# Kernel tuning notes

Measured on AMD Instinct MI355X. Metric: run time of the kernel, lower is better.

The kernel has to match this reference:

```python
import jax, jax.numpy as jnp
import numpy as np
from jax import lax

B = 32          # batch
L = 12          # n_blocks
HD = 768        # hidden_d
NH = 12         # n_heads
DH = HD // NH   # d_head = 64
NP = 14         # n_patches per side
S = NP * NP + 1 # seq len = 197
IN_D = 32 * 25  # 800, conv channels * 5x5 patch
OUT = 1000
EPS = 1e-5


def setup_inputs() -> dict:
    key = jax.random.key(0)
    ks = jax.random.split(key, 10)
    r = lambda k, s: jax.random.normal(k, s, jnp.float32) * 0.02
    return {
        "images": jax.random.normal(ks[0], (B, 3, 280, 280), jnp.float32),
        "conv_w": r(ks[1], (32, 3, 5, 5)),
        "conv_b": jnp.zeros((32,), jnp.float32),
        "bn_g": jnp.ones((32,), jnp.float32),
        "bn_b": jnp.zeros((32,), jnp.float32),
        "bn_m": jnp.zeros((32,), jnp.float32),
        "bn_v": jnp.ones((32,), jnp.float32),
        "map_w": r(ks[2], (HD, IN_D)),
        "map_b": jnp.zeros((HD,), jnp.float32),
        "cls_tok": jax.random.uniform(ks[3], (1, HD), jnp.float32),
        "ln_g": jnp.ones((L, HD), jnp.float32),
        "ln_b": jnp.zeros((L, HD), jnp.float32),
        "wq": r(ks[4], (L, NH, DH, DH)), "bq": jnp.zeros((L, NH, DH), jnp.float32),
        "wk": r(ks[5], (L, NH, DH, DH)), "bk": jnp.zeros((L, NH, DH), jnp.float32),
        "wv": r(ks[6], (L, NH, DH, DH)), "bv": jnp.zeros((L, NH, DH), jnp.float32),
        "mlp_w": r(ks[7], (OUT, HD)),
        "mlp_b": jnp.zeros((OUT,), jnp.float32),
    }


def _pos_emb(s, d):
    # pe[i,j] = sin(i/10000^(j/d)) if j even else cos(i/10000^((j-1)/d))
    i = jnp.arange(s, dtype=jnp.float32)[:, None]
    j = jnp.arange(d)[None, :]
    jf = j.astype(jnp.float32)
    ang_even = i / (10000.0 ** (jf / d))
    ang_odd = i / (10000.0 ** ((jf - 1.0) / d))
    return jnp.where(j % 2 == 0, jnp.sin(ang_even), jnp.cos(ang_odd))


def reference(images, conv_w, conv_b, bn_g, bn_b, bn_m, bn_v, map_w, map_b,
              cls_tok, ln_g, ln_b, wq, bq, wk, bk, wv, bv, mlp_w, mlp_b):
    # patch-embed conv: (B,3,280,280) -> (B,32,70,70)
    x = lax.conv_general_dilated(images, conv_w, (4, 4), [(1, 1), (1, 1)],
                                 dimension_numbers=('NCHW', 'OIHW', 'NCHW'))
    x = x + conv_b[None, :, None, None]
    # BatchNorm (eval) + ReLU; Dropout is identity in eval
    x = (x - bn_m[None, :, None, None]) * (bn_g / jnp.sqrt(bn_v + EPS))[None, :, None, None] \
        + bn_b[None, :, None, None]
    x = jax.nn.relu(x)
    n = x.shape[0]
    # split into 5x5 patches: (n,32,70,70) -> (n,196,800)
    x = x.reshape(n, 32, NP, 5, NP, 5).transpose(0, 2, 4, 1, 3, 5).reshape(n, NP * NP, IN_D)
    tok = x @ map_w.T + map_b                                   # (n,196,768)
    tok = jnp.concatenate([jnp.broadcast_to(cls_tok[None], (n, 1, HD)), tok], axis=1)
    out = tok + _pos_emb(S, HD)[None]                           # (n,197,768)
    scale = 1.0 / jnp.sqrt(jnp.float32(DH))
    for l in range(L):
        # LayerNorm
        mu = out.mean(-1, keepdims=True)
        var = out.var(-1, keepdims=True)
        h = (out - mu) / jnp.sqrt(var + EPS) * ln_g[l] + ln_b[l]
        xh = h.reshape(n, S, NH, DH)
        q = jnp.einsum('nshd,hed->nshe', xh, wq[l]) + bq[l]
        k = jnp.einsum('nshd,hed->nshe', xh, wk[l]) + bk[l]
        v = jnp.einsum('nshd,hed->nshe', xh, wv[l]) + bv[l]
        attn = jax.nn.softmax(jnp.einsum('nshe,nthe->nhst', q, k) * scale, axis=-1)
        o = jnp.einsum('nhst,nthe->nshe', attn, v).reshape(n, S, HD)
        out = out + o  # residual; NOTE: source block has no MLP sublayer
    cls = out[:, 0]
    return jax.nn.softmax(cls @ mlp_w.T + mlp_b, axis=-1)
```

## Files before the change

kernel.cpp:

```cpp
#include <hip/hip_runtime.h>

#define BB 32
#define LLAYERS 12
#define HDIM 768
#define NHEAD 12
#define DHEAD 64
#define SEQ 197
#define IND 800
#define NOUT 1000
#define EPSF 1e-5f
#define NTOK (BB * SEQ)
#define NPATCH (BB * 196)
#define SCALE 0.125f

typedef __attribute__((ext_vector_type(4))) float f32x4;
typedef __attribute__((ext_vector_type(8))) short short8;

static __device__ __forceinline__ ushort f2bf(float f) {
    union { float f; unsigned u; } v; v.f = f;
    unsigned r = v.u + 0x7FFFu + ((v.u >> 16) & 1u);
    return (ushort)(r >> 16);
}

static __device__ __forceinline__ void gload_lds16(const void* g, void* l) {
    __builtin_amdgcn_global_load_lds(
        (const __attribute__((address_space(1))) void*)g,
        (__attribute__((address_space(3))) void*)l, 16, 0, 0);
}

__global__ __launch_bounds__(256) void k_cvt(
    const float* __restrict__ s, ushort* __restrict__ d, int n4)
{
    int i = blockIdx.x * 256 + threadIdx.x;
    if (i < n4) {
        float4 v = *(const float4*)&s[i * 4];
        ushort4 u = {f2bf(v.x), f2bf(v.y), f2bf(v.z), f2bf(v.w)};
        *(ushort4*)&d[i * 4] = u;
    }
}

__global__ __launch_bounds__(256) void k_cvtw(
    const float* __restrict__ wq, const float* __restrict__ wk,
    const float* __restrict__ wv, ushort* __restrict__ dst)
{
    int t = blockIdx.x * 256 + threadIdx.x;
    if (t >= 3 * 144 * 512) return;
    int lane = t & 63;
    int rest = t >> 6;
    int ktnt = rest & 7;
    int mlh = rest >> 3;
    int h = mlh % 12, ml = mlh / 12;
    int l = ml % 12, m = ml / 12;
    int nt = ktnt & 3, kt = ktnt >> 2;
    int e = nt * 16 + (lane & 15);
    int d = kt * 32 + (lane >> 4) * 8;
    const float* src = ((m == 0) ? wq : (m == 1) ? wk : wv)
                       + (((long)l * 12 + h) * 64 + e) * 64 + d;
    float4 a = *(const float4*)src;
    float4 b = *(const float4*)(src + 4);
    short8 u;
    u[0] = (short)f2bf(a.x); u[1] = (short)f2bf(a.y);
    u[2] = (short)f2bf(a.z); u[3] = (short)f2bf(a.w);
    u[4] = (short)f2bf(b.x); u[5] = (short)f2bf(b.y);
    u[6] = (short)f2bf(b.z); u[7] = (short)f2bf(b.w);
    *(short8*)&dst[(long)mlh * 4096 + ktnt * 512 + lane * 8] = u;
}

__global__ __launch_bounds__(256) void k_pos(float* __restrict__ pos)
{
    int s = blockIdx.x;
    for (int e = threadIdx.x; e < HDIM; e += 256) {
        float freq = expf((float)(e & ~1) * (-9.210340371976184f / 768.0f));
        float ang = (float)s * freq;
        pos[s * HDIM + e] = (e & 1) ? cosf(ang) : sinf(ang);
    }
}

__global__ __launch_bounds__(320) void k_conv_patch(
    const float* __restrict__ img, const float* __restrict__ cw,
    const float* __restrict__ cb, const float* __restrict__ bg,
    const float* __restrict__ bbias, const float* __restrict__ bm,
    const float* __restrict__ bvv, ushort* __restrict__ X)
{
    __shared__ float tile[2][3][21][21];
    __shared__ float w[2400];
    __shared__ float scale[32], shift[32];
    int tid = threadIdx.x;

    for (int i = tid; i < 2400; i += 320) w[i] = cw[i];
    if (tid < 32) {
        float sc = bg[tid] * rsqrtf(bvv[tid] + EPSF);
        scale[tid] = sc;
        shift[tid] = (cb[tid] - bm[tid]) * sc + bbias[tid];
    }
    for (int i = tid; i < 2 * 3 * 441; i += 320) {
        int pp = i / 1323, j = i % 1323;
        int c = j / 441, r = (j / 21) % 21, cc = j % 21;
        int gp = blockIdx.x * 2 + pp;
        int n = gp / 196, p = gp % 196;
        int h0 = (p / 14) * 20 - 1, w0 = (p % 14) * 20 - 1;
        int gh = h0 + r, gw = w0 + cc;
        float v = 0.f;
        if (gh >= 0 && gh < 280 && gw >= 0 && gw < 280)
            v = img[((long)(n * 3 + c) * 280 + gh) * 280 + gw];
        tile[pp][c][r][cc] = v;
    }
    __syncthreads();

    int pp = tid / 160, u = tid % 160;
    int c = u / 5, ph = u % 5;
    float acc[5] = {0.f, 0.f, 0.f, 0.f, 0.f};
    const float* wp = &w[c * 75];
    #pragma unroll
    for (int ci = 0; ci < 3; ci++) {
        #pragma unroll
        for (int kh = 0; kh < 5; kh++) {
            const float* row = &tile[pp][ci][ph * 4 + kh][0];
            float rv[21];
            #pragma unroll
            for (int j = 0; j < 21; j++) rv[j] = row[j];
            #pragma unroll
            for (int kw = 0; kw < 5; kw++) {
                float wv = wp[ci * 25 + kh * 5 + kw];
                #pragma unroll
                for (int pw = 0; pw < 5; pw++)
                    acc[pw] += rv[pw * 4 + kw] * wv;
            }
        }
    }
    int gp = blockIdx.x * 2 + pp;
    long ob = (long)gp * 800 + c * 25 + ph * 5;
    #pragma unroll
    for (int pw = 0; pw < 5; pw++) {
        float val = acc[pw] * scale[c] + shift[c];
        X[ob + pw] = f2bf(fmaxf(val, 0.f));
    }
}

__global__ void k_cls(const float* __restrict__ cls_tok,
                      const float* __restrict__ pos, float* __restrict__ tok)
{
    int n = blockIdx.x, tid = threadIdx.x;
    for (int e = tid; e < HDIM; e += 256)
        tok[(long)n * SEQ * HDIM + e] = cls_tok[e] + pos[e];
}

__global__ __launch_bounds__(256, 2) void k_embed(
    const ushort* __restrict__ Xg, const ushort* __restrict__ Wg,
    const float* __restrict__ bias, const float* __restrict__ pos,
    float* __restrict__ tok)
{
    __shared__ __align__(16) ushort As[128 * 32];
    __shared__ __align__(16) ushort Bs[64 * 32];
    int m0 = blockIdx.x * 128, e0 = blockIdx.y * 64;
    int tid = threadIdx.x, lane = tid & 63, wave = tid >> 6;
    int col = lane & 15, quad = lane >> 4;
    int wm = (wave & 1) * 64, wn = (wave >> 1) * 32;
    int lr = lane >> 2, lc = (lane & 3) * 8;
    f32x4 zero4 = {0.f, 0.f, 0.f, 0.f};
    f32x4 acc[4][2];
    #pragma unroll
    for (int mt = 0; mt < 4; mt++)
        #pragma unroll
        for (int nt = 0; nt < 2; nt++) acc[mt][nt] = zero4;

    for (int k0 = 0; k0 < 800; k0 += 32) {
        __syncthreads();
        #pragma unroll
        for (int i = 0; i < 2; i++) {
            int c = wave * 2 + i;
            gload_lds16(&Xg[(long)(m0 + c * 16 + lr) * 800 + k0 + lc], &As[c * 512]);
        }
        {
            int c = wave;
            gload_lds16(&Wg[(long)(e0 + c * 16 + lr) * 800 + k0 + lc], &Bs[c * 512]);
        }
        __syncthreads();
        short8 a[4], b[2];
        #pragma unroll
        for (int mt = 0; mt < 4; mt++)
            a[mt] = *(const short8*)&As[(wm + mt * 16 + col) * 32 + quad * 8];
        #pragma unroll
        for (int nt = 0; nt < 2; nt++)
            b[nt] = *(const short8*)&Bs[(wn + nt * 16 + col) * 32 + quad * 8];
        #pragma unroll
        for (int mt = 0; mt < 4; mt++)
            #pragma unroll
            for (int nt = 0; nt < 2; nt++)
                acc[mt][nt] = __builtin_amdgcn_mfma_f32_16x16x32_bf16(a[mt], b[nt], acc[mt][nt], 0, 0, 0);
    }
    #pragma unroll
    for (int mt = 0; mt < 4; mt++) {
        #pragma unroll
        for (int r = 0; r < 4; r++) {
            int m = m0 + wm + mt * 16 + quad * 4 + r;
            int n = m / 196, s = m - n * 196 + 1;
            long rowb = ((long)n * SEQ + s) * HDIM;
            #pragma unroll
            for (int nt = 0; nt < 2; nt++) {
                int e = e0 + wn + nt * 16 + col;
                tok[rowb + e] = acc[mt][nt][r] + bias[e] + pos[s * HDIM + e];
            }
        }
    }
}

__global__ __launch_bounds__(256) void k_lnstats0(
    const float* __restrict__ tok, float* __restrict__ stats_out)
{
    int tid = threadIdx.x, lane = tid & 63, wave = tid >> 6;
    int row = blockIdx.x * 4 + wave;
    const float* p = tok + (long)row * HDIM;
    float s = 0.f, sq = 0.f;
    #pragma unroll
    for (int k = 0; k < 3; k++) {
        float4 v = *(const float4*)&p[k * 256 + lane * 4];
        s += v.x + v.y + v.z + v.w;
        sq += v.x * v.x + v.y * v.y + v.z * v.z + v.w * v.w;
    }
    #pragma unroll
    for (int off = 1; off < 64; off <<= 1) {
        s += __shfl_xor(s, off);
        sq += __shfl_xor(sq, off);
    }
    float* sp = &stats_out[(long)row * 24];
    if (lane == 0) { sp[0] = s; sp[1] = sq; }
    if (lane >= 2 && lane < 24) sp[lane] = 0.f;
}

__global__ __launch_bounds__(512, 1) void k_layer(
    float* __restrict__ tok,
    const float* __restrict__ stats_in, float* __restrict__ stats_out,
    const float* __restrict__ lng, const float* __restrict__ lnb,
    const ushort* __restrict__ wqs, const float* __restrict__ bqp,
    const ushort* __restrict__ wks, const float* __restrict__ bkp,
    const ushort* __restrict__ wvs, const float* __restrict__ bvp)
{
    __shared__ __align__(16) ushort Wl[3][4096];
    __shared__ __align__(16) ushort xh[208 * 72];
    __shared__ __align__(16) ushort Ks[208 * 72];
    __shared__ __align__(16) ushort Vt[64 * 232];
    __shared__ __align__(16) ushort Ps[8][16 * 40];
    __shared__ float smu[208], srstd[208];
    __shared__ float bias[3][64];

    int h = blockIdx.x, n = blockIdx.y;
    int tid = threadIdx.x, lane = tid & 63, wave = tid >> 6;
    int col = lane & 15, quad = lane >> 4;
    f32x4 zero4 = {0.f, 0.f, 0.f, 0.f};

    const ushort* wsz0 = wqs + (long)h * 4096;
    const ushort* wsz1 = wks + (long)h * 4096;
    const ushort* wsz2 = wvs + (long)h * 4096;
    {
        int c = wave;
        gload_lds16(&wsz0[c * 512 + lane * 8], &Wl[0][c * 512]);
        gload_lds16(&wsz1[c * 512 + lane * 8], &Wl[1][c * 512]);
        gload_lds16(&wsz2[c * 512 + lane * 8], &Wl[2][c * 512]);
    }
    if (tid < 192) {
        int m = tid >> 6, e = tid & 63;
        bias[m][e] = ((m == 0) ? bqp : (m == 1) ? bkp : bvp)[h * 64 + e];
    }
    for (int r = tid; r < SEQ; r += 512) {
        const float* sp = &stats_in[((long)n * SEQ + r) * 24];
        float s = 0.f, sq = 0.f;
        #pragma unroll
        for (int j = 0; j < 6; j++) {
            float4 v = *(const float4*)&sp[j * 4];
            s += v.x + v.z;
            sq += v.y + v.w;
        }
        float mu = s / 768.f;
        smu[r] = mu;
        srstd[r] = rsqrtf(sq / 768.f - mu * mu + EPSF);
    }
    for (int i = tid; i < 64 * 24; i += 512) {
        int e = i / 24, t = 208 + i % 24;
        Vt[e * 232 + t] = 0;
    }
    __syncthreads();

    for (int i = tid; i < 208 * 16; i += 512) {
        int r = i >> 4, c4 = i & 15;
        ushort4 u = {0, 0, 0, 0};
        if (r < SEQ) {
            float4 v = *(const float4*)&tok[((long)n * SEQ + r) * HDIM + h * 64 + c4 * 4];
            float mu = smu[r], rstd = srstd[r];
            int d = c4 * 4;
            const float* g = &lng[h * 64 + d];
            const float* bb = &lnb[h * 64 + d];
            u.x = f2bf((v.x - mu) * rstd * g[0] + bb[0]);
            u.y = f2bf((v.y - mu) * rstd * g[1] + bb[1]);
            u.z = f2bf((v.z - mu) * rstd * g[2] + bb[2]);
            u.w = f2bf((v.w - mu) * rstd * g[3] + bb[3]);
        }
        *(ushort4*)&xh[r * 72 + c4 * 4] = u;
    }
    __syncthreads();

    #pragma unroll
    for (int sl = 0; sl < 2; sl++) {
        int st = sl * 8 + wave;
        if (st < 13) {
            int q0 = st * 16;
            short8 a[2];
            a[0] = *(const short8*)&xh[(q0 + col) * 72 + quad * 8];
            a[1] = *(const short8*)&xh[(q0 + col) * 72 + 32 + quad * 8];
            #pragma unroll
            for (int m = 0; m < 3; m++) {
                f32x4 acc[4] = {zero4, zero4, zero4, zero4};
                #pragma unroll
                for (int kt = 0; kt < 2; kt++)
                    #pragma unroll
                    for (int nt = 0; nt < 4; nt++) {
                        short8 b = *(const short8*)&Wl[m][(kt * 4 + nt) * 512 + lane * 8];
                        acc[nt] = __builtin_amdgcn_mfma_f32_16x16x32_bf16(a[kt], b, acc[nt], 0, 0, 0);
                    }
                if (m == 0) {
                    #pragma unroll
                    for (int nt = 0; nt < 4; nt++)
                        #pragma unroll
                        for (int r = 0; r < 4; r++)
                            xh[(q0 + quad * 4 + r) * 72 + nt * 16 + col] =
                                f2bf(acc[nt][r] + bias[0][nt * 16 + col]);
                } else if (m == 1) {
                    #pragma unroll
                    for (int nt = 0; nt < 4; nt++)
                        #pragma unroll
                        for (int r = 0; r < 4; r++)
                            Ks[(q0 + quad * 4 + r) * 72 + nt * 16 + col] =
                                f2bf(acc[nt][r] + bias[1][nt * 16 + col]);
                } else {
                    #pragma unroll
                    for (int nt = 0; nt < 4; nt++)
                        #pragma unroll
                        for (int r = 0; r < 4; r++)
                            Vt[(nt * 16 + col) * 232 + q0 + quad * 4 + r] =
                                f2bf(acc[nt][r] + bias[2][nt * 16 + col]);
                }
            }
        }
    }
    __syncthreads();

    ushort* myP = &Ps[wave][0];
    #pragma unroll
    for (int sl = 0; sl < 2; sl++) {
        int st = sl * 8 + wave;
        if (st >= 13) continue;
        int q0 = st * 16;
        short8 aq[2];
        aq[0] = *(const short8*)&xh[(q0 + col) * 72 + quad * 8];
        aq[1] = *(const short8*)&xh[(q0 + col) * 72 + 32 + quad * 8];

        f32x4 sc[13];
        #pragma unroll
        for (int tt = 0; tt < 13; tt++) sc[tt] = zero4;
        #pragma unroll
        for (int tt = 0; tt < 13; tt++) {
            #pragma unroll
            for (int dt = 0; dt < 2; dt++) {
                short8 bk = *(const short8*)&Ks[(tt * 16 + col) * 72 + dt * 32 + quad * 8];
                sc[tt] = __builtin_amdgcn_mfma_f32_16x16x32_bf16(aq[dt], bk, sc[tt], 0, 0, 0);
            }
        }

        float rinv[4];
        #pragma unroll
        for (int r = 0; r < 4; r++) {
            float m = -1e30f;
            #pragma unroll
            for (int tt = 0; tt < 12; tt++) m = fmaxf(m, sc[tt][r]);
            if (col < 5) m = fmaxf(m, sc[12][r]);
            #pragma unroll
            for (int off = 1; off < 16; off <<= 1) m = fmaxf(m, __shfl_xor(m, off));
            float s = 0.f;
            #pragma unroll
            for (int tt = 0; tt < 12; tt++) {
                float e = __expf((sc[tt][r] - m) * SCALE);
                sc[tt][r] = e; s += e;
            }
            float e12 = (col < 5) ? __expf((sc[12][r] - m) * SCALE) : 0.f;
            sc[12][r] = e12; s += e12;
            #pragma unroll
            for (int off = 1; off < 16; off <<= 1) s += __shfl_xor(s, off);
            rinv[r] = 1.f / s;
        }

        f32x4 oacc[4];
        #pragma unroll
        for (int nt = 0; nt < 4; nt++) oacc[nt] = zero4;
        #pragma unroll
        for (int kt = 0; kt < 7; kt++) {
            #pragma unroll
            for (int half = 0; half < 2; half++) {
                int tt = kt * 2 + half;
                #pragma unroll
                for (int r = 0; r < 4; r++) {
                    float v = (tt < 13) ? sc[tt][r] : 0.f;
                    myP[(quad * 4 + r) * 40 + half * 16 + col] = f2bf(v);
                }
            }
            short8 pa = *(const short8*)&myP[col * 40 + quad * 8];
            #pragma unroll
            for (int nt = 0; nt < 4; nt++) {
                short8 vb = *(const short8*)&Vt[(nt * 16 + col) * 232 + kt * 32 + quad * 8];
                oacc[nt] = __builtin_amdgcn_mfma_f32_16x16x32_bf16(pa, vb, oacc[nt], 0, 0, 0);
            }
        }

        #pragma unroll
        for (int r = 0; r < 4; r++) {
            int row = q0 + quad * 4 + r;
            float s = 0.f, sq = 0.f;
            if (row < SEQ) {
                float rv = rinv[r];
                #pragma unroll
                for (int nt = 0; nt < 4; nt++) {
                    long o = ((long)n * SEQ + row) * HDIM + h * 64 + nt * 16 + col;
                    float nv = tok[o] + oacc[nt][r] * rv;
                    tok[o] = nv;
                    s += nv; sq += nv * nv;
                }
            }
            #pragma unroll
            for (int off = 1; off < 16; off <<= 1) {
                s += __shfl_xor(s, off);
                sq += __shfl_xor(sq, off);
            }
            if (row < SEQ && col == 0) {
                float* sp = &stats_out[((long)n * SEQ + row) * 24 + h * 2];
                sp[0] = s; sp[1] = sq;
            }
        }
    }
}

__global__ __launch_bounds__(256) void k_logits(
    const float* __restrict__ tok, const float* __restrict__ W,
    const float* __restrict__ b, float* __restrict__ logits)
{
    int n = blockIdx.x, oc = blockIdx.y;
    int tid = threadIdx.x, lane = tid & 63, wave = tid >> 6;
    const float* cp = &tok[(long)n * SEQ * HDIM];
    float4 c0 = *(const float4*)&cp[lane * 4];
    float4 c1 = *(const float4*)&cp[256 + lane * 4];
    float4 c2 = *(const float4*)&cp[512 + lane * 4];
    int obeg = oc * 125, oend = obeg + 125;
    for (int o = obeg + wave; o < oend; o += 4) {
        const float* wr = &W[(long)o * HDIM];
        float4 w0 = *(const float4*)&wr[lane * 4];
        float4 w1 = *(const float4*)&wr[256 + lane * 4];
        float4 w2 = *(const float4*)&wr[512 + lane * 4];
        float s = c0.x * w0.x + c0.y * w0.y + c0.z * w0.z + c0.w * w0.w
                + c1.x * w1.x + c1.y * w1.y + c1.z * w1.z + c1.w * w1.w
                + c2.x * w2.x + c2.y * w2.y + c2.z * w2.z + c2.w * w2.w;
        #pragma unroll
        for (int off = 1; off < 64; off <<= 1) s += __shfl_xor(s, off);
        if (lane == 0) logits[n * NOUT + o] = s + b[o];
    }
}

__global__ __launch_bounds__(256) void k_smax(
    const float* __restrict__ logits, float* __restrict__ out)
{
    __shared__ float lg[NOUT];
    __shared__ float red[256];
    int n = blockIdx.x, tid = threadIdx.x;
    for (int o = tid; o < NOUT; o += 256) lg[o] = logits[n * NOUT + o];
    __syncthreads();
    float m = -1e30f;
    for (int o = tid; o < NOUT; o += 256) m = fmaxf(m, lg[o]);
    red[tid] = m; __syncthreads();
    for (int off = 128; off > 0; off >>= 1) {
        if (tid < off) red[tid] = fmaxf(red[tid], red[tid + off]);
        __syncthreads();
    }
    float mx = red[0];
    __syncthreads();
    float s = 0.f;
    for (int o = tid; o < NOUT; o += 256) {
        float e = __expf(lg[o] - mx);
        lg[o] = e; s += e;
    }
    red[tid] = s; __syncthreads();
    for (int off = 128; off > 0; off >>= 1) {
        if (tid < off) red[tid] += red[tid + off];
        __syncthreads();
    }
    float inv = 1.f / red[0];
    for (int o = tid; o < NOUT; o += 256) out[(long)n * NOUT + o] = lg[o] * inv;
}

extern "C" void kernel_launch(void* const* d_in, const int* in_sizes, int n_in,
                              void* d_out, int out_size, void* d_ws, size_t ws_size,
                              hipStream_t stream)
{
    const float* images  = (const float*)d_in[0];
    const float* conv_w  = (const float*)d_in[1];
    const float* conv_b  = (const float*)d_in[2];
    const float* bn_g    = (const float*)d_in[3];
    const float* bn_b    = (const float*)d_in[4];
    const float* bn_m    = (const float*)d_in[5];
    const float* bn_v    = (const float*)d_in[6];
    const float* map_w   = (const float*)d_in[7];
    const float* map_b   = (const float*)d_in[8];
    const float* cls_tok = (const float*)d_in[9];
    const float* ln_g    = (const float*)d_in[10];
    const float* ln_b    = (const float*)d_in[11];
    const float* wq      = (const float*)d_in[12];
    const float* bq      = (const float*)d_in[13];
    const float* wk      = (const float*)d_in[14];
    const float* bk      = (const float*)d_in[15];
    const float* wv      = (const float*)d_in[16];
    const float* bv      = (const float*)d_in[17];
    const float* mlp_w   = (const float*)d_in[18];
    const float* mlp_b   = (const float*)d_in[19];
    float* out = (float*)d_out;

    const long SZ_X   = (long)NPATCH * IND;
    const long SZ_W   = (long)HDIM * IND;
    const long SZ_WS  = (long)3 * 144 * 4096;
    const long SZ_POS = (long)SEQ * HDIM;
    const long SZ_TOK = (long)NTOK * HDIM;
    const long SZ_ST  = (long)NTOK * 24;

    ushort* Xbf   = (ushort*)d_ws;
    ushort* Wbf   = Xbf + SZ_X;
    ushort* Wswz  = Wbf + SZ_W;
    float*  pos   = (float*)(Wswz + SZ_WS);
    float*  tok   = pos + SZ_POS;
    float*  sta   = tok + SZ_TOK;
    float*  stb   = sta + SZ_ST;
    float* logits = (float*)Xbf;

    k_cvt<<<600, 256, 0, stream>>>(map_w, Wbf, (int)(SZ_W / 4));
    k_cvtw<<<(3 * 144 * 512 + 255) / 256, 256, 0, stream>>>(wq, wk, wv, Wswz);
    k_pos<<<SEQ, 256, 0, stream>>>(pos);
    k_conv_patch<<<NPATCH / 2, 320, 0, stream>>>(images, conv_w, conv_b, bn_g,
                                                 bn_b, bn_m, bn_v, Xbf);
    k_cls<<<BB, 256, 0, stream>>>(cls_tok, pos, tok);
    dim3 ge(49, 12);
    k_embed<<<ge, 256, 0, stream>>>(Xbf, Wbf, map_b, pos, tok);

    k_lnstats0<<<NTOK / 4, 256, 0, stream>>>(tok, sta);
    for (int l = 0; l < LLAYERS; l++) {
        float* srd = (l & 1) ? stb : sta;
        float* swr = (l & 1) ? sta : stb;
        dim3 gl(12, 32);
        k_layer<<<gl, 512, 0, stream>>>(tok, srd, swr,
            ln_g + (long)l * HDIM, ln_b + (long)l * HDIM,
            Wswz + (long)(0 * 144 + l * 12) * 4096, bq + (long)l * NHEAD * DHEAD,
            Wswz + (long)(1 * 144 + l * 12) * 4096, bk + (long)l * NHEAD * DHEAD,
            Wswz + (long)(2 * 144 + l * 12) * 4096, bv + (long)l * NHEAD * DHEAD);
    }
    dim3 glo(BB, 8);
    k_logits<<<glo, 256, 0, stream>>>(tok, mlp_w, mlp_b, logits);
    k_smax<<<BB, 256, 0, stream>>>(logits, out);
}
```

Baseline: 624.5 us.

## Drop weight and xh LDS staging to fit more blocks per CU

Removes the LDS copies of the QKV weights and the normalized-input tile. Each wave now builds its LayerNorm A-fragments directly in registers from global memory and loads weight fragments straight from global (L2). Q is routed through the per-wave P scratch buffer and held in registers for the attention phase, and one block-wide barrier is dropped. Launch bounds change to 4 blocks per CU to use the lower LDS footprint, at the cost of higher register pressure (a, aq and b arrays) and more global weight reads per wave.

```diff
diff --git a/kernel.cpp b/kernel.cpp
--- a/kernel.cpp
+++ b/kernel.cpp
@@ -228,7 +228,7 @@
     if (lane >= 2 && lane < 24) sp[lane] = 0.f;
 }
 
-__global__ __launch_bounds__(512, 1) void k_layer(
+__global__ __launch_bounds__(512, 4) void k_layer(
     float* __restrict__ tok,
     const float* __restrict__ stats_in, float* __restrict__ stats_out,
     const float* __restrict__ lng, const float* __restrict__ lnb,
@@ -236,31 +236,25 @@
     const ushort* __restrict__ wks, const float* __restrict__ bkp,
     const ushort* __restrict__ wvs, const float* __restrict__ bvp)
 {
-    __shared__ __align__(16) ushort Wl[3][4096];
-    __shared__ __align__(16) ushort xh[208 * 72];
     __shared__ __align__(16) ushort Ks[208 * 72];
     __shared__ __align__(16) ushort Vt[64 * 232];
-    __shared__ __align__(16) ushort Ps[8][16 * 40];
+    __shared__ __align__(16) ushort Ps[8][16 * 72];
     __shared__ float smu[208], srstd[208];
     __shared__ float bias[3][64];
+    __shared__ float lngs[64], lnbs[64];
 
     int h = blockIdx.x, n = blockIdx.y;
     int tid = threadIdx.x, lane = tid & 63, wave = tid >> 6;
     int col = lane & 15, quad = lane >> 4;
     f32x4 zero4 = {0.f, 0.f, 0.f, 0.f};
 
-    const ushort* wsz0 = wqs + (long)h * 4096;
-    const ushort* wsz1 = wks + (long)h * 4096;
-    const ushort* wsz2 = wvs + (long)h * 4096;
-    {
-        int c = wave;
-        gload_lds16(&wsz0[c * 512 + lane * 8], &Wl[0][c * 512]);
-        gload_lds16(&wsz1[c * 512 + lane * 8], &Wl[1][c * 512]);
-        gload_lds16(&wsz2[c * 512 + lane * 8], &Wl[2][c * 512]);
-    }
     if (tid < 192) {
         int m = tid >> 6, e = tid & 63;
         bias[m][e] = ((m == 0) ? bqp : (m == 1) ? bkp : bvp)[h * 64 + e];
+    } else if (tid < 256) {
+        lngs[tid - 192] = lng[h * 64 + tid - 192];
+    } else if (tid < 320) {
+        lnbs[tid - 256] = lnb[h * 64 + tid - 256];
     }
     for (int r = tid; r < SEQ; r += 512) {
         const float* sp = &stats_in[((long)n * SEQ + r) * 24];
@@ -281,78 +275,88 @@
     }
     __syncthreads();
 
-    for (int i = tid; i < 208 * 16; i += 512) {
-        int r = i >> 4, c4 = i & 15;
-        ushort4 u = {0, 0, 0, 0};
-        if (r < SEQ) {
-            float4 v = *(const float4*)&tok[((long)n * SEQ + r) * HDIM + h * 64 + c4 * 4];
-            float mu = smu[r], rstd = srstd[r];
-            int d = c4 * 4;
-            const float* g = &lng[h * 64 + d];
-            const float* bb = &lnb[h * 64 + d];
-            u.x = f2bf((v.x - mu) * rstd * g[0] + bb[0]);
-            u.y = f2bf((v.y - mu) * rstd * g[1] + bb[1]);
-            u.z = f2bf((v.z - mu) * rstd * g[2] + bb[2]);
-            u.w = f2bf((v.w - mu) * rstd * g[3] + bb[3]);
-        }
-        *(ushort4*)&xh[r * 72 + c4 * 4] = u;
-    }
-    __syncthreads();
-
+    long tokb = (long)n * SEQ * HDIM + h * 64;
+    short8 a[2][2];
     #pragma unroll
     for (int sl = 0; sl < 2; sl++) {
         int st = sl * 8 + wave;
-        if (st < 13) {
+        if (st >= 13) continue;
+        int row = st * 16 + col; if (row > SEQ - 1) row = SEQ - 1;
+        float mu = smu[row], rs = srstd[row];
+        #pragma unroll
+        for (int kt = 0; kt < 2; kt++) {
+            const float* tp = &tok[tokb + (long)row * HDIM + kt * 32 + quad * 8];
+            float4 v0 = *(const float4*)tp;
+            float4 v1 = *(const float4*)(tp + 4);
+            const float* g = &lngs[kt * 32 + quad * 8];
+            const float* bb = &lnbs[kt * 32 + quad * 8];
+            short8 u;
+            u[0] = (short)f2bf((v0.x - mu) * rs * g[0] + bb[0]);
+            u[1] = (short)f2bf((v0.y - mu) * rs * g[1] + bb[1]);
+            u[2] = (short)f2bf((v0.z - mu) * rs * g[2] + bb[2]);
+            u[3] = (short)f2bf((v0.w - mu) * rs * g[3] + bb[3]);
+            u[4] = (short)f2bf((v1.x - mu) * rs * g[4] + bb[4]);
+            u[5] = (short)f2bf((v1.y - mu) * rs * g[5] + bb[5]);
+            u[6] = (short)f2bf((v1.z - mu) * rs * g[6] + bb[6]);
+            u[7] = (short)f2bf((v1.w - mu) * rs * g[7] + bb[7]);
+            a[sl][kt] = u;
+        }
+    }
+
+    ushort* myP = &Ps[wave][0];
+    short8 aq[2][2];
+    #pragma unroll
+    for (int m = 0; m < 3; m++) {
+        const ushort* wp = ((m == 0) ? wqs : (m == 1) ? wks : wvs) + (long)h * 4096;
+        short8 b[8];
+        #pragma unroll
+        for (int f = 0; f < 8; f++)
+            b[f] = *(const short8*)&wp[f * 512 + lane * 8];
+        #pragma unroll
+        for (int sl = 0; sl < 2; sl++) {
+            int st = sl * 8 + wave;
+            if (st >= 13) continue;
             int q0 = st * 16;
-            short8 a[2];
-            a[0] = *(const short8*)&xh[(q0 + col) * 72 + quad * 8];
-            a[1] = *(const short8*)&xh[(q0 + col) * 72 + 32 + quad * 8];
-            #pragma unroll
-            for (int m = 0; m < 3; m++) {
-                f32x4 acc[4] = {zero4, zero4, zero4, zero4};
+            f32x4 acc[4] = {zero4, zero4, zero4, zero4};
+            #pragma unroll
+            for (int kt = 0; kt < 2; kt++)
+                #pragma unroll
+                for (int nt = 0; nt < 4; nt++)
+                    acc[nt] = __builtin_amdgcn_mfma_f32_16x16x32_bf16(a[sl][kt], b[kt * 4 + nt], acc[nt], 0, 0, 0);
+            if (m == 0) {
+                #pragma unroll
+                for (int nt = 0; nt < 4; nt++)
+                    #pragma unroll
+                    for (int r = 0; r < 4; r++)
+                        myP[(quad * 4 + r) * 72 + nt * 16 + col] =
+                            f2bf(acc[nt][r] + bias[0][nt * 16 + col]);
                 #pragma unroll
                 for (int kt = 0; kt < 2; kt++)
+                    aq[sl][kt] = *(const short8*)&myP[col * 72 + kt * 32 + quad * 8];
+            } else if (m == 1) {
+                #pragma unroll
+                for (int nt = 0; nt < 4; nt++)
                     #pragma unroll
-                    for (int nt = 0; nt < 4; nt++) {
-                        short8 b = *(const short8*)&Wl[m][(kt * 4 + nt) * 512 + lane * 8];
-                        acc[nt] = __builtin_amdgcn_mfma_f32_16x16x32_bf16(a[kt], b, acc[nt], 0, 0, 0);
-                    }
-                if (m == 0) {
+                    for (int r = 0; r < 4; r++)
+                        Ks[(q0 + quad * 4 + r) * 72 + nt * 16 + col] =
+                            f2bf(acc[nt][r] + bias[1][nt * 16 + col]);
+            } else {
+                #pragma unroll
+                for (int nt = 0; nt < 4; nt++)
                     #pragma unroll
-                    for (int nt = 0; nt < 4; nt++)
-                        #pragma unroll
-                        for (int r = 0; r < 4; r++)
-                            xh[(q0 + quad * 4 + r) * 72 + nt * 16 + col] =
-                                f2bf(acc[nt][r] + bias[0][nt * 16 + col]);
-                } else if (m == 1) {
-                    #pragma unroll
-                    for (int nt = 0; nt < 4; nt++)
-                        #pragma unroll
-                        for (int r = 0; r < 4; r++)
-                            Ks[(q0 + quad * 4 + r) * 72 + nt * 16 + col] =
-                                f2bf(acc[nt][r] + bias[1][nt * 16 + col]);
-                } else {
-                    #pragma unroll
-                    for (int nt = 0; nt < 4; nt++)
-                        #pragma unroll
-                        for (int r = 0; r < 4; r++)
-                            Vt[(nt * 16 + col) * 232 + q0 + quad * 4 + r] =
-                                f2bf(acc[nt][r] + bias[2][nt * 16 + col]);
-                }
+                    for (int r = 0; r < 4; r++)
+                        Vt[(nt * 16 + col) * 232 + q0 + quad * 4 + r] =
+                            f2bf(acc[nt][r] + bias[2][nt * 16 + col]);
             }
         }
     }
     __syncthreads();
 
-    ushort* myP = &Ps[wave][0];
     #pragma unroll
     for (int sl = 0; sl < 2; sl++) {
         int st = sl * 8 + wave;
         if (st >= 13) continue;
         int q0 = st * 16;
-        short8 aq[2];
-        aq[0] = *(const short8*)&xh[(q0 + col) * 72 + quad * 8];
-        aq[1] = *(const short8*)&xh[(q0 + col) * 72 + 32 + quad * 8];
 
         f32x4 sc[13];
         #pragma unroll
@@ -362,7 +366,7 @@
             #pragma unroll
             for (int dt = 0; dt < 2; dt++) {
                 short8 bk = *(const short8*)&Ks[(tt * 16 + col) * 72 + dt * 32 + quad * 8];
-                sc[tt] = __builtin_amdgcn_mfma_f32_16x16x32_bf16(aq[dt], bk, sc[tt], 0, 0, 0);
+                sc[tt] = __builtin_amdgcn_mfma_f32_16x16x32_bf16(aq[sl][dt], bk, sc[tt], 0, 0, 0);
             }
         }
 
@@ -399,10 +403,10 @@
                 #pragma unroll
                 for (int r = 0; r < 4; r++) {
                     float v = (tt < 13) ? sc[tt][r] : 0.f;
-                    myP[(quad * 4 + r) * 40 + half * 16 + col] = f2bf(v);
+                    myP[(quad * 4 + r) * 72 + half * 16 + col] = f2bf(v);
                 }
             }
-            short8 pa = *(const short8*)&myP[col * 40 + quad * 8];
+            short8 pa = *(const short8*)&myP[col * 72 + quad * 8];
             #pragma unroll
             for (int nt = 0; nt < 4; nt++) {
                 short8 vb = *(const short8*)&Vt[(nt * 16 + col) * 232 + kt * 32 + quad * 8];
```

After: 523.1 us. 1.19x faster.
